# Kernel optimization log

Measured on AMD Instinct MI355X. Metric: run time of the kernel, lower is better.

Reference implementation:

```python
import jax, jax.numpy as jnp
import numpy as np

V, R, A, C, T = 10000, 5, 8, 64, 64
EPS = 1e-3  # keras BatchNormalization default epsilon


def setup_inputs() -> dict:
    key = jax.random.key(0)
    ks = jax.random.split(key, 8)
    signal = jax.random.normal(ks[0], (V, C), dtype=jnp.float32)
    bc_idx = jax.random.randint(ks[1], (V, R, A, 3), 0, V, dtype=jnp.int32)
    bc_w = jax.random.uniform(ks[2], (V, R, A, 3), dtype=jnp.float32)
    bc_w = bc_w / jnp.sum(bc_w, axis=-1, keepdims=True)  # barycentric weights sum to 1
    scale = 0.05
    templates1 = jax.random.normal(ks[3], (T, R, A, C), dtype=jnp.float32) * scale
    bias1 = jax.random.normal(ks[4], (T,), dtype=jnp.float32) * scale
    templates2 = jax.random.normal(ks[5], (T, R, A, T), dtype=jnp.float32) * scale
    bias2 = jax.random.normal(ks[6], (T,), dtype=jnp.float32) * scale
    return {
        "signal": signal,
        "bc_w": bc_w,
        "templates1": templates1,
        "bias1": bias1,
        "gamma1": jnp.ones((T,), jnp.float32),
        "beta1": jnp.zeros((T,), jnp.float32),
        "templates2": templates2,
        "bias2": bias2,
        "gamma2": jnp.ones((T,), jnp.float32),
        "beta2": jnp.zeros((T,), jnp.float32),
        "bc_idx": bc_idx,
    }


def _conv_dirac(sig, bc_idx, bc_w, templates, bias):
    # Barycentric interpolation (the 'patch operator'): gather 3 mesh-vertex
    # signals per template point and blend. gathered: (V, R, A, 3, Cin)
    gathered = sig[bc_idx]
    interp = jnp.einsum("vraic,vrai->vrac", gathered, bc_w)  # (V, R, A, Cin)
    # All A rotations of the template along the angular axis:
    # rolled signal[a] = interp[(a - o) % A]  <=>  contract with templates[(a + o) % A].
    rot = (jnp.arange(A)[:, None] + jnp.arange(A)[None, :]) % A  # (O, A)
    t_rot = templates[:, :, rot, :]  # (T, R, O, A, Cin)
    return jnp.einsum("vrac,troac->vot", interp, t_rot) + bias  # (V, O, T)


def _angular_max_pool(x):
    # Pick, per vertex, the rotation with maximal Euclidean response norm.
    idx = jnp.argmax(jnp.linalg.norm(x, axis=-1), axis=1)  # (V,)
    return jnp.take_along_axis(x, idx[:, None, None], axis=1)[:, 0, :]  # (V, T)


def _bn_inference(x, gamma, beta):
    # Fresh BN at inference: moving_mean = 0, moving_var = 1.
    inv = jax.lax.rsqrt(jnp.asarray(1.0 + EPS, x.dtype))
    return gamma * (x * inv) + beta


def reference(signal, bc_w, templates1, bias1, gamma1, beta1,
              templates2, bias2, gamma2, beta2, bc_idx):
    s = _conv_dirac(signal, bc_idx, bc_w, templates1, bias1)
    s = jax.nn.relu(_bn_inference(_angular_max_pool(s), gamma1, beta1))
    s = _conv_dirac(s, bc_idx, bc_w, templates2, bias2)
    s = _bn_inference(_angular_max_pool(s), gamma2, beta2)
    # input_dim == amt_templates -> identity shortcut (no rescale branch)
    return jax.nn.relu(s + signal)
```

## Files before the change

kernel.cpp:

```cpp
#include <hip/hip_runtime.h>

#define NVV 10000
#define NKSTEPS 80
#define KSPLIT 40
#define BN_INV 0.99950037468777316f

#define AS1 __attribute__((address_space(1)))
#define AS3 __attribute__((address_space(3)))

typedef float f32x4 __attribute__((ext_vector_type(4)));
typedef short short8 __attribute__((ext_vector_type(8)));
typedef unsigned short ushort;

#define ACH_USH 5120
#define ACH_B   10240
#define WCH_B   16384

__device__ __forceinline__ ushort bsplit(float v, float& rem) {
    unsigned u = __float_as_uint(v);
    unsigned r = (u + 0x7fffu + ((u >> 16) & 1u)) & 0xffff0000u;
    rem = v - __uint_as_float(r);
    return (ushort)(r >> 16);
}

__device__ __forceinline__ void interp_store2(ushort* __restrict__ dstp, int it,
                                              const float4& g0, const float4& g1, const float4& g2,
                                              float w0, float w1, float w2) {
    const int m = it >> 3, kq = it & 7;
    const float av[4] = {g0.x, g0.y, g0.z, g0.w};
    const float bv[4] = {g1.x, g1.y, g1.z, g1.w};
    const float cv[4] = {g2.x, g2.y, g2.z, g2.w};
    ushort h1[4], h2[4];
    #pragma unroll
    for (int e = 0; e < 4; ++e) {
        const float vv = w0 * av[e] + w1 * bv[e] + w2 * cv[e];
        float r1, r2;
        h1[e] = bsplit(vv, r1); h2[e] = bsplit(r1, r2);
    }
    const int mt = m >> 4, mm = m & 15, qk = kq >> 1, hf = kq & 1;
    const int o0 = ((mt * 2 + 0) * 4 + qk) * 128 + mm * 8 + hf * 4;
    *(uint2*)(dstp + o0)       = make_uint2((unsigned)h1[0] | ((unsigned)h1[1] << 16),
                                            (unsigned)h1[2] | ((unsigned)h1[3] << 16));
    *(uint2*)(dstp + o0 + 512) = make_uint2((unsigned)h2[0] | ((unsigned)h2[1] << 16),
                                            (unsigned)h2[2] | ((unsigned)h2[3] << 16));
}

__global__ void build_w_kernel(const float* __restrict__ t1,
                               const float* __restrict__ t2,
                               ushort* __restrict__ W1g,
                               ushort* __restrict__ W2g) {
    const int k = blockIdx.x;
    const int n = threadIdx.x;
    const float* T  = blockIdx.y ? t2 : t1;
    ushort*      Wg = blockIdx.y ? W2g : W1g;
    const int r = k >> 9, a = (k >> 6) & 7, c = k & 63;
    const int o = n >> 6, t = n & 63;
    const float w = T[((t * 5 + r) * 8 + ((o + a) & 7)) * 64 + c];
    float r1, r2;
    const ushort h1 = bsplit(w, r1);
    const ushort h2 = bsplit(r1, r2);
    const int kstep = k >> 5, kw = k & 31, q = kw >> 3, kk = kw & 7;
    const int strip = n >> 7, nl = n & 127, nt = nl >> 4, l16 = nl & 15;
    const size_t base = (size_t)(kstep * 4 + strip) * 8192;
    const int off = ((nt * 2 + 0) * 4 + q) * 128 + l16 * 8 + kk;
    Wg[base + off]       = h1;
    Wg[base + off + 512] = h2;
}

__global__ void interp_kernel(const float* __restrict__ src,
                              const int*   __restrict__ bc_idx,
                              const float* __restrict__ bc_w,
                              ushort*      __restrict__ Ag,
                              int mg0) {
    const int cid = blockIdx.x;
    const int mgl = cid / NKSTEPS;
    const int ks  = cid % NKSTEPS;
    const int mg  = mg0 + mgl;
    const int x   = threadIdx.x;
    ushort* chunk = Ag + (size_t)cid * ACH_USH;
    const int ra = ks >> 1;
    #pragma unroll
    for (int s = 0; s < 3; ++s) {
        const int it = x + 256 * s;
        if (it < 640) {
            const int m = it >> 3, kq = it & 7;
            const int v = mg * 80 + m;
            const int*   ip = bc_idx + v * 120 + ra * 3;
            const float* wp = bc_w  + v * 120 + ra * 3;
            const int c0 = (ks & 1) * 32 + kq * 4;
            const float4 g0 = *(const float4*)(src + (size_t)ip[0] * 64 + c0);
            const float4 g1 = *(const float4*)(src + (size_t)ip[1] * 64 + c0);
            const float4 g2 = *(const float4*)(src + (size_t)ip[2] * 64 + c0);
            interp_store2(chunk, it, g0, g1, g2, wp[0], wp[1], wp[2]);
        }
    }
}

__global__ __launch_bounds__(256, 3)
void gemm_kernel(const ushort* __restrict__ Ag,
                 const ushort* __restrict__ Wg,
                 float*       __restrict__ S1,
                 float*       __restrict__ S2,
                 int mg0, int Pp, int mpx) {
    __shared__ ushort sW[2][8192];
    __shared__ ushort sA[2][ACH_USH];
    const int x = threadIdx.x;
    const int b = blockIdx.x;
    const int xcd   = b & 7;
    const int rest  = b >> 3;
    const int khalf = rest & 1;
    const int strip = (rest >> 1) & 3;
    const int mgl_l = rest >> 3;
    const int mg_local = xcd * mpx + mgl_l;
    if (mg_local >= Pp) return;
    const int mg    = mg0 + mg_local;
    const int Mbase = mg * 80;
    const int ks0   = khalf * KSPLIT;
    const int wj  = x >> 6;
    const int l16 = x & 15;
    const int q   = (x & 63) >> 4;

    f32x4 d[5][2] = {};

    const char* gWb = (const char*)Wg;
    const char* gAb = (const char*)Ag + (size_t)mg_local * NKSTEPS * ACH_B;

    {
        const char* gw = gWb + (size_t)(ks0 * 4 + strip) * WCH_B;
        char*       lw = (char*)sW[0];
        #pragma unroll
        for (int j = 0; j < 4; ++j)
            __builtin_amdgcn_global_load_lds((AS1 const void*)(gw + (x + 256 * j) * 16),
                                             (AS3 void*)(lw + (x + 256 * j) * 16), 16, 0, 0);
        const char* ga = gAb + (size_t)ks0 * ACH_B;
        char*       la = (char*)sA[0];
        #pragma unroll
        for (int j = 0; j < 3; ++j) {
            const int it = x + 256 * j;
            if (it < 640)
                __builtin_amdgcn_global_load_lds((AS1 const void*)(ga + it * 16),
                                                 (AS3 void*)(la + it * 16), 16, 0, 0);
        }
    }
    __syncthreads();

    for (int ki = 0; ki < KSPLIT; ++ki) {
        const int ks = ks0 + ki;
        const int cur = ki & 1, nxt = cur ^ 1;
        if (ki + 1 < KSPLIT) {
            const char* gw = gWb + (size_t)((ks + 1) * 4 + strip) * WCH_B;
            char*       lw = (char*)sW[nxt];
            #pragma unroll
            for (int j = 0; j < 4; ++j)
                __builtin_amdgcn_global_load_lds((AS1 const void*)(gw + (x + 256 * j) * 16),
                                                 (AS3 void*)(lw + (x + 256 * j) * 16), 16, 0, 0);
            const char* ga = gAb + (size_t)(ks + 1) * ACH_B;
            char*       la = (char*)sA[nxt];
            #pragma unroll
            for (int j = 0; j < 3; ++j) {
                const int it = x + 256 * j;
                if (it < 640)
                    __builtin_amdgcn_global_load_lds((AS1 const void*)(ga + it * 16),
                                                     (AS3 void*)(la + it * 16), 16, 0, 0);
            }
        }

        short8 w1f[2], w2f[2];
        #pragma unroll
        for (int nt = 0; nt < 2; ++nt) {
            const int ntg = 2 * wj + nt;
            w1f[nt] = *(const short8*)(sW[cur] + ((ntg * 2 + 0) * 4 + q) * 128 + l16 * 8);
            w2f[nt] = *(const short8*)(sW[cur] + ((ntg * 2 + 1) * 4 + q) * 128 + l16 * 8);
        }
        #pragma unroll
        for (int mt = 0; mt < 5; ++mt) {
            const short8 a1 = *(const short8*)(sA[cur] + ((mt * 2 + 0) * 4 + q) * 128 + l16 * 8);
            const short8 a2 = *(const short8*)(sA[cur] + ((mt * 2 + 1) * 4 + q) * 128 + l16 * 8);
            #pragma unroll
            for (int nt = 0; nt < 2; ++nt) {
                d[mt][nt] = __builtin_amdgcn_mfma_f32_16x16x32_bf16(a1, w1f[nt], d[mt][nt], 0, 0, 0);
                d[mt][nt] = __builtin_amdgcn_mfma_f32_16x16x32_bf16(a1, w2f[nt], d[mt][nt], 0, 0, 0);
                d[mt][nt] = __builtin_amdgcn_mfma_f32_16x16x32_bf16(a2, w1f[nt], d[mt][nt], 0, 0, 0);
            }
        }
        __syncthreads();
    }

    float* Sh = khalf ? S2 : S1;
    #pragma unroll
    for (int mt = 0; mt < 5; ++mt) {
        #pragma unroll
        for (int nt = 0; nt < 2; ++nt) {
            #pragma unroll
            for (int r = 0; r < 4; ++r) {
                const int mglob = Mbase + mt * 16 + q * 4 + r;
                const int nglob = strip * 128 + wj * 32 + nt * 16 + l16;
                Sh[(size_t)mglob * 512 + nglob] = d[mt][nt][r];
            }
        }
    }
}

template<bool RES>
__global__ void pool_kernel(const float* __restrict__ S1,
                            const float* __restrict__ S2,
                            const float* __restrict__ bias,
                            const float* __restrict__ gamma,
                            const float* __restrict__ beta,
                            const float* __restrict__ resid,
                            float*       __restrict__ dst) {
    const int w = threadIdx.x >> 6;
    const int t = threadIdx.x & 63;
    const int v = blockIdx.x * 4 + w;
    const float bt = bias[t];
    float vals[8], n2[8];
    #pragma unroll
    for (int o = 0; o < 8; ++o) {
        const size_t idx = (size_t)v * 512 + o * 64 + t;
        const float val = S1[idx] + S2[idx] + bt;
        vals[o] = val;
        float s = val * val;
        #pragma unroll
        for (int off = 1; off < 64; off <<= 1) s += __shfl_xor(s, off, 64);
        n2[o] = s;
    }
    int bj = 0; float bv = n2[0];
    #pragma unroll
    for (int j = 1; j < 8; ++j) {
        if (n2[j] > bv) { bv = n2[j]; bj = j; }
    }
    float val = vals[0];
    #pragma unroll
    for (int j = 1; j < 8; ++j) val = (bj == j) ? vals[j] : val;
    float r = gamma[t] * (val * BN_INV) + beta[t];
    if (RES) r += resid[(size_t)v * 64 + t];
    dst[(size_t)v * 64 + t] = fmaxf(r, 0.0f);
}

extern "C" void kernel_launch(void* const* d_in, const int* in_sizes, int n_in,
                              void* d_out, int out_size, void* d_ws, size_t ws_size,
                              hipStream_t stream) {
    const float* signal = (const float*)d_in[0];
    const float* bc_w   = (const float*)d_in[1];
    const float* t1     = (const float*)d_in[2];
    const float* bias1  = (const float*)d_in[3];
    const float* gamma1 = (const float*)d_in[4];
    const float* beta1  = (const float*)d_in[5];
    const float* t2     = (const float*)d_in[6];
    const float* bias2  = (const float*)d_in[7];
    const float* gamma2 = (const float*)d_in[8];
    const float* beta2  = (const float*)d_in[9];
    const int*   bc_idx = (const int*)d_in[10];

    const size_t WSTG = (size_t)NKSTEPS * 4 * 8192;
    ushort* W1g = (ushort*)d_ws;
    ushort* W2g = W1g + WSTG;
    float* S1 = (float*)(W2g + WSTG);
    float* S2 = S1 + (size_t)NVV * 512;
    float* s1 = S2 + (size_t)NVV * 512;
    ushort* Ag = (ushort*)(s1 + (size_t)NVV * 64);
    float* out = (float*)d_out;

    const size_t used  = (size_t)((char*)Ag - (char*)d_ws);
    const size_t avail = ws_size > used ? ws_size - used : 0;
    int P = (int)(avail / ((size_t)NKSTEPS * ACH_B));
    if (P > 125) P = 125;
    if (P < 1)  P = 1;

    build_w_kernel<<<dim3(2560, 2), 512, 0, stream>>>(t1, t2, W1g, W2g);

    for (int mg0 = 0; mg0 < 125; mg0 += P) {
        const int Pp  = (125 - mg0 < P) ? (125 - mg0) : P;
        const int mpx = (Pp + 7) / 8;
        interp_kernel<<<Pp * NKSTEPS, 256, 0, stream>>>(signal, bc_idx, bc_w, Ag, mg0);
        gemm_kernel<<<64 * mpx, 256, 0, stream>>>(Ag, W1g, S1, S2, mg0, Pp, mpx);
    }
    pool_kernel<false><<<2500, 256, 0, stream>>>(S1, S2, bias1, gamma1, beta1, nullptr, s1);

    for (int mg0 = 0; mg0 < 125; mg0 += P) {
        const int Pp  = (125 - mg0 < P) ? (125 - mg0) : P;
        const int mpx = (Pp + 7) / 8;
        interp_kernel<<<Pp * NKSTEPS, 256, 0, stream>>>(s1, bc_idx, bc_w, Ag, mg0);
        gemm_kernel<<<64 * mpx, 256, 0, stream>>>(Ag, W2g, S1, S2, mg0, Pp, mpx);
    }
    pool_kernel<true><<<2500, 256, 0, stream>>>(S1, S2, bias2, gamma2, beta2, signal, out);
}
```

Measured before the change: 359.0 us.

## Load GEMM fragments straight into registers and widen block to full N

The GEMM kernel no longer stages A and W chunks through LDS with async global-to-LDS copies and barriers. Each wave now loads its A and W fragments directly from global memory into registers, double-buffered across k-steps, and computes a 80x128 slice of N. One block covers all 512 output columns for its M group, so the grid shrinks to 2 blocks per M group. This removes LDS traffic and barriers, but uses many more registers (occupancy 1), has every wave reload the same A fragments from global/L2, and leaves far fewer blocks to fill the GPU.

```diff
diff --git a/kernel.cpp b/kernel.cpp
--- a/kernel.cpp
+++ b/kernel.cpp
@@ -96,105 +96,77 @@
     }
 }
 
-__global__ __launch_bounds__(256, 3)
+#define GEMM_LOADS(AB, WB, KS)                                              \
+    if ((KS) < ksend) {                                                     \
+        const AS1 char* an = aBase + (size_t)(KS) * ACH_B;                  \
+        const AS1 char* wn = wBase + (size_t)(KS) * (4 * WCH_B);            \
+        _Pragma("unroll")                                                   \
+        for (int f = 0; f < 10; ++f)                                        \
+            AB[f] = *(const AS1 short8*)(an + f * 1024);                    \
+        _Pragma("unroll")                                                   \
+        for (int f = 0; f < 16; ++f)                                        \
+            WB[f] = *(const AS1 short8*)(wn + f * 1024);                    \
+    }
+
+#define GEMM_MFMAS(AB, WB)                                                  \
+    _Pragma("unroll")                                                       \
+    for (int mt = 0; mt < 5; ++mt) {                                        \
+        _Pragma("unroll")                                                   \
+        for (int nt = 0; nt < 8; ++nt) {                                    \
+            d[mt][nt] = __builtin_amdgcn_mfma_f32_16x16x32_bf16(            \
+                AB[mt * 2 + 0], WB[nt * 2 + 0], d[mt][nt], 0, 0, 0);        \
+            d[mt][nt] = __builtin_amdgcn_mfma_f32_16x16x32_bf16(            \
+                AB[mt * 2 + 0], WB[nt * 2 + 1], d[mt][nt], 0, 0, 0);        \
+            d[mt][nt] = __builtin_amdgcn_mfma_f32_16x16x32_bf16(            \
+                AB[mt * 2 + 1], WB[nt * 2 + 0], d[mt][nt], 0, 0, 0);        \
+        }                                                                   \
+    }
+
+__global__ __launch_bounds__(256, 1)
 void gemm_kernel(const ushort* __restrict__ Ag,
                  const ushort* __restrict__ Wg,
                  float*       __restrict__ S1,
                  float*       __restrict__ S2,
-                 int mg0, int Pp, int mpx) {
-    __shared__ ushort sW[2][8192];
-    __shared__ ushort sA[2][ACH_USH];
+                 int mg0) {
+    const int b = blockIdx.x;
+    const int mgl   = b >> 1;
+    const int khalf = b & 1;
+    const int Mbase = (mg0 + mgl) * 80;
     const int x = threadIdx.x;
-    const int b = blockIdx.x;
-    const int xcd   = b & 7;
-    const int rest  = b >> 3;
-    const int khalf = rest & 1;
-    const int strip = (rest >> 1) & 3;
-    const int mgl_l = rest >> 3;
-    const int mg_local = xcd * mpx + mgl_l;
-    if (mg_local >= Pp) return;
-    const int mg    = mg0 + mg_local;
-    const int Mbase = mg * 80;
+    const int wj   = x >> 6;
+    const int lane = x & 63;
+    const int l16  = lane & 15;
+    const int q    = lane >> 4;
     const int ks0   = khalf * KSPLIT;
-    const int wj  = x >> 6;
-    const int l16 = x & 15;
-    const int q   = (x & 63) >> 4;
-
-    f32x4 d[5][2] = {};
-
-    const char* gWb = (const char*)Wg;
-    const char* gAb = (const char*)Ag + (size_t)mg_local * NKSTEPS * ACH_B;
-
-    {
-        const char* gw = gWb + (size_t)(ks0 * 4 + strip) * WCH_B;
-        char*       lw = (char*)sW[0];
-        #pragma unroll
-        for (int j = 0; j < 4; ++j)
-            __builtin_amdgcn_global_load_lds((AS1 const void*)(gw + (x + 256 * j) * 16),
-                                             (AS3 void*)(lw + (x + 256 * j) * 16), 16, 0, 0);
-        const char* ga = gAb + (size_t)ks0 * ACH_B;
-        char*       la = (char*)sA[0];
-        #pragma unroll
-        for (int j = 0; j < 3; ++j) {
-            const int it = x + 256 * j;
-            if (it < 640)
-                __builtin_amdgcn_global_load_lds((AS1 const void*)(ga + it * 16),
-                                                 (AS3 void*)(la + it * 16), 16, 0, 0);
-        }
-    }
-    __syncthreads();
-
-    for (int ki = 0; ki < KSPLIT; ++ki) {
-        const int ks = ks0 + ki;
-        const int cur = ki & 1, nxt = cur ^ 1;
-        if (ki + 1 < KSPLIT) {
-            const char* gw = gWb + (size_t)((ks + 1) * 4 + strip) * WCH_B;
-            char*       lw = (char*)sW[nxt];
-            #pragma unroll
-            for (int j = 0; j < 4; ++j)
-                __builtin_amdgcn_global_load_lds((AS1 const void*)(gw + (x + 256 * j) * 16),
-                                                 (AS3 void*)(lw + (x + 256 * j) * 16), 16, 0, 0);
-            const char* ga = gAb + (size_t)(ks + 1) * ACH_B;
-            char*       la = (char*)sA[nxt];
-            #pragma unroll
-            for (int j = 0; j < 3; ++j) {
-                const int it = x + 256 * j;
-                if (it < 640)
-                    __builtin_amdgcn_global_load_lds((AS1 const void*)(ga + it * 16),
-                                                     (AS3 void*)(la + it * 16), 16, 0, 0);
-            }
-        }
-
-        short8 w1f[2], w2f[2];
-        #pragma unroll
-        for (int nt = 0; nt < 2; ++nt) {
-            const int ntg = 2 * wj + nt;
-            w1f[nt] = *(const short8*)(sW[cur] + ((ntg * 2 + 0) * 4 + q) * 128 + l16 * 8);
-            w2f[nt] = *(const short8*)(sW[cur] + ((ntg * 2 + 1) * 4 + q) * 128 + l16 * 8);
-        }
-        #pragma unroll
-        for (int mt = 0; mt < 5; ++mt) {
-            const short8 a1 = *(const short8*)(sA[cur] + ((mt * 2 + 0) * 4 + q) * 128 + l16 * 8);
-            const short8 a2 = *(const short8*)(sA[cur] + ((mt * 2 + 1) * 4 + q) * 128 + l16 * 8);
-            #pragma unroll
-            for (int nt = 0; nt < 2; ++nt) {
-                d[mt][nt] = __builtin_amdgcn_mfma_f32_16x16x32_bf16(a1, w1f[nt], d[mt][nt], 0, 0, 0);
-                d[mt][nt] = __builtin_amdgcn_mfma_f32_16x16x32_bf16(a1, w2f[nt], d[mt][nt], 0, 0, 0);
-                d[mt][nt] = __builtin_amdgcn_mfma_f32_16x16x32_bf16(a2, w1f[nt], d[mt][nt], 0, 0, 0);
-            }
-        }
-        __syncthreads();
+    const int ksend = ks0 + KSPLIT;
+
+    f32x4 d[5][8] = {};
+
+    const AS1 char* aBase = (const AS1 char*)Ag
+        + (size_t)mgl * NKSTEPS * ACH_B + lane * 16;
+    const AS1 char* wBase = (const AS1 char*)Wg
+        + (size_t)wj * WCH_B + lane * 16;
+
+    short8 A0[10], W0[16], A1[10], W1[16];
+
+    GEMM_LOADS(A0, W0, ks0);
+
+    for (int ks = ks0; ks < ksend; ks += 2) {
+        GEMM_LOADS(A1, W1, ks + 1);
+        GEMM_MFMAS(A0, W0);
+        GEMM_LOADS(A0, W0, ks + 2);
+        GEMM_MFMAS(A1, W1);
     }
 
     float* Sh = khalf ? S2 : S1;
     #pragma unroll
     for (int mt = 0; mt < 5; ++mt) {
         #pragma unroll
-        for (int nt = 0; nt < 2; ++nt) {
+        for (int nt = 0; nt < 8; ++nt) {
             #pragma unroll
             for (int r = 0; r < 4; ++r) {
                 const int mglob = Mbase + mt * 16 + q * 4 + r;
-                const int nglob = strip * 128 + wj * 32 + nt * 16 + l16;
+                const int nglob = wj * 128 + nt * 16 + l16;
                 Sh[(size_t)mglob * 512 + nglob] = d[mt][nt][r];
             }
         }
@@ -270,18 +242,16 @@
     build_w_kernel<<<dim3(2560, 2), 512, 0, stream>>>(t1, t2, W1g, W2g);
 
     for (int mg0 = 0; mg0 < 125; mg0 += P) {
-        const int Pp  = (125 - mg0 < P) ? (125 - mg0) : P;
-        const int mpx = (Pp + 7) / 8;
+        const int Pp = (125 - mg0 < P) ? (125 - mg0) : P;
         interp_kernel<<<Pp * NKSTEPS, 256, 0, stream>>>(signal, bc_idx, bc_w, Ag, mg0);
-        gemm_kernel<<<64 * mpx, 256, 0, stream>>>(Ag, W1g, S1, S2, mg0, Pp, mpx);
+        gemm_kernel<<<2 * Pp, 256, 0, stream>>>(Ag, W1g, S1, S2, mg0);
     }
     pool_kernel<false><<<2500, 256, 0, stream>>>(S1, S2, bias1, gamma1, beta1, nullptr, s1);
 
     for (int mg0 = 0; mg0 < 125; mg0 += P) {
-        const int Pp  = (125 - mg0 < P) ? (125 - mg0) : P;
-        const int mpx = (Pp + 7) / 8;
+        const int Pp = (125 - mg0 < P) ? (125 - mg0) : P;
         interp_kernel<<<Pp * NKSTEPS, 256, 0, stream>>>(s1, bc_idx, bc_w, Ag, mg0);
-        gemm_kernel<<<64 * mpx, 256, 0, stream>>>(Ag, W2g, S1, S2, mg0, Pp, mpx);
+        gemm_kernel<<<2 * Pp, 256, 0, stream>>>(Ag, W2g, S1, S2, mg0);
     }
     pool_kernel<true><<<2500, 256, 0, stream>>>(S1, S2, bias2, gamma2, beta2, signal, out);
 }
```

New measurement: 314.3 us. 12.4% less time.
